# Kernel optimization log

Hardware: AMD Instinct MI355X
Metric: run time of the kernel (lower is better)

Reference implementation:

```python
import jax, jax.numpy as jnp
import numpy as np

N, E, F, H, C, G = 50000, 600000, 128, 128, 10, 500
NUM_GIN = 3
BN_EPS = 1e-5


def _bn(x, gamma, beta):
    # BatchNorm1d in training mode: batch statistics over node/graph dim
    m = jnp.mean(x, axis=0)
    v = jnp.mean((x - m) ** 2, axis=0)
    return (x - m) * jax.lax.rsqrt(v + BN_EPS) * gamma + beta


def setup_inputs() -> dict:
    key = jax.random.key(0)
    ks = jax.random.split(key, 16)
    s = 1.0 / np.sqrt(H)
    inp = {
        "x": jax.random.normal(ks[0], (N, F), dtype=jnp.float32),
        "edge_index": jax.random.randint(ks[1], (2, E), 0, N),
        "batch": jnp.sort(jax.random.randint(ks[2], (N,), 0, G)),
        # bn_feat
        "gamma_feat": jnp.ones((F,), jnp.float32),
        "beta_feat": jnp.full((F,), 1e-4, jnp.float32),
        # conv_feat (GCNConv gfn=True -> pure linear)
        "W_feat": jax.random.uniform(ks[3], (F, H), jnp.float32, -s, s),
        "b_feat": jnp.zeros((H,), jnp.float32),
        # GIN conv MLPs, stacked over 3 layers
        "gin_W1": jax.random.uniform(ks[4], (NUM_GIN, H, H), jnp.float32, -s, s),
        "gin_b1": jnp.zeros((NUM_GIN, H), jnp.float32),
        "gin_gamma": jnp.ones((NUM_GIN, H), jnp.float32),
        "gin_beta": jnp.full((NUM_GIN, H), 1e-4, jnp.float32),
        "gin_W2": jax.random.uniform(ks[5], (NUM_GIN, H, H), jnp.float32, -s, s),
        "gin_b2": jnp.zeros((NUM_GIN, H), jnp.float32),
        # one FC block (num_fc_layers=2 -> 1 bn+lin)
        "gamma_fc": jnp.ones((H,), jnp.float32),
        "beta_fc": jnp.full((H,), 1e-4, jnp.float32),
        "W_fc": jax.random.uniform(ks[6], (H, H), jnp.float32, -s, s),
        "b_fc": jnp.zeros((H,), jnp.float32),
        # bn_hidden + classifier
        "gamma_h": jnp.ones((H,), jnp.float32),
        "beta_h": jnp.full((H,), 1e-4, jnp.float32),
        "W_cls": jax.random.uniform(ks[7], (H, C), jnp.float32, -s, s),
        "b_cls": jnp.zeros((C,), jnp.float32),
    }
    return inp


def reference(x, gamma_feat, beta_feat, W_feat, b_feat,
              gin_W1, gin_b1, gin_gamma, gin_beta, gin_W2, gin_b2,
              gamma_fc, beta_fc, W_fc, b_fc,
              gamma_h, beta_h, W_cls, b_cls,
              edge_index, batch):
    src, dst = edge_index[0], edge_index[1]
    h = _bn(x, gamma_feat, beta_feat)
    h = jax.nn.relu(h @ W_feat + b_feat)  # GCNConv gfn=True == Linear
    for i in range(NUM_GIN):
        # GIN aggregation: (1+eps)*x + sum_{j->i} x_j, eps=0
        agg = jnp.zeros_like(h).at[dst].add(h[src])
        z = h + agg
        z = jax.nn.relu(_bn(z @ gin_W1[i] + gin_b1[i], gin_gamma[i], gin_beta[i]))
        h = jax.nn.relu(z @ gin_W2[i] + gin_b2[i])
    g = jax.ops.segment_sum(h, batch, num_segments=G)  # global_add_pool -> [G,H]
    g = jax.nn.relu(_bn(g, gamma_fc, beta_fc) @ W_fc + b_fc)
    g = _bn(g, gamma_h, beta_h)
    logits = g @ W_cls + b_cls
    return jax.nn.log_softmax(logits, axis=-1)
```

## Files before the change

### kernel.cpp

```cpp
#include <hip/hip_runtime.h>
#include <math.h>

#define N_NODES 50000
#define N_EDGES 600000
#define HDIM 128
#define NCLS 10
#define NGRAPH 500
#define BN_EPS 1e-5f
#define SCAN_BLOCKS 196

typedef short bf16x8 __attribute__((ext_vector_type(8)));
typedef float f32x4 __attribute__((ext_vector_type(4)));

__global__ void colstats_kernel(const float* __restrict__ X, int M, float* __restrict__ stats) {
    int col = threadIdx.x & 127;
    int sub = threadIdx.x >> 7;
    float s = 0.f, sq = 0.f;
    for (int r = blockIdx.x * 2 + sub; r < M; r += gridDim.x * 2) {
        float v = X[(size_t)r * HDIM + col];
        s += v; sq += v * v;
    }
    atomicAdd(&stats[col], s);
    atomicAdd(&stats[HDIM + col], sq);
}

__global__ void hist_kernel(const int* __restrict__ ei, int* __restrict__ counts) {
    int e = blockIdx.x * 256 + threadIdx.x;
    if (e < N_EDGES) atomicAdd(&counts[ei[N_EDGES + e]], 1);
}

__global__ __launch_bounds__(256) void scan1_kernel(const int* __restrict__ counts,
                                                    int* __restrict__ partial,
                                                    int* __restrict__ blockSums) {
    __shared__ int tmp[256];
    int tid = threadIdx.x;
    int i = blockIdx.x * 256 + tid;
    int v = (i < N_NODES) ? counts[i] : 0;
    tmp[tid] = v;
    __syncthreads();
#pragma unroll
    for (int off = 1; off < 256; off <<= 1) {
        int t = (tid >= off) ? tmp[tid - off] : 0;
        __syncthreads();
        tmp[tid] += t;
        __syncthreads();
    }
    if (i < N_NODES) partial[i] = tmp[tid] - v;
    if (tid == 255) blockSums[blockIdx.x] = tmp[255];
}

__global__ __launch_bounds__(256) void scan2_kernel(const int* __restrict__ blockSums,
                                                    int* __restrict__ blockBase) {
    __shared__ int tmp[256];
    int tid = threadIdx.x;
    int v = (tid < SCAN_BLOCKS) ? blockSums[tid] : 0;
    tmp[tid] = v;
    __syncthreads();
#pragma unroll
    for (int off = 1; off < 256; off <<= 1) {
        int t = (tid >= off) ? tmp[tid - off] : 0;
        __syncthreads();
        tmp[tid] += t;
        __syncthreads();
    }
    if (tid < SCAN_BLOCKS) blockBase[tid] = tmp[tid] - v;
}

__global__ __launch_bounds__(256) void scan3_kernel(const int* __restrict__ partial,
                                                    const int* __restrict__ blockBase,
                                                    int* __restrict__ offsets,
                                                    int* __restrict__ cursor) {
    int i = blockIdx.x * 256 + threadIdx.x;
    if (i < N_NODES) {
        int o = partial[i] + blockBase[blockIdx.x];
        offsets[i] = o;
        cursor[i] = o;
    }
    if (i == 0) offsets[N_NODES] = N_EDGES;
}

__global__ void fill_kernel(const int* __restrict__ ei, int* __restrict__ cursor, int* __restrict__ csr) {
    int e = blockIdx.x * 256 + threadIdx.x;
    if (e < N_EDGES) {
        int d = ei[N_EDGES + e];
        int pos = atomicAdd(&cursor[d], 1);
        csr[pos] = ei[e];
    }
}

__global__ __launch_bounds__(256) void agg_kernel(const float* __restrict__ h,
                                                  const int* __restrict__ offsets,
                                                  const int* __restrict__ csr,
                                                  float* __restrict__ z) {
    int node = (blockIdx.x * 256 + threadIdx.x) >> 6;
    int lane = threadIdx.x & 63;
    if (node >= N_NODES) return;
    int c0 = lane * 2;
    int beg = offsets[node], end = offsets[node + 1];
    const float2 self = *(const float2*)&h[(size_t)node * HDIM + c0];
    float ax = self.x, ay = self.y;
    for (int j = beg; j < end; j += 64) {
        int cnt = min(64, end - j);
        int sl = (j + lane < end) ? csr[j + lane] : 0;
        int t = 0;
        for (; t + 4 <= cnt; t += 4) {
            int s0 = __shfl(sl, t, 64);
            int s1 = __shfl(sl, t + 1, 64);
            int s2 = __shfl(sl, t + 2, 64);
            int s3 = __shfl(sl, t + 3, 64);
            float2 v0 = *(const float2*)&h[(size_t)s0 * HDIM + c0];
            float2 v1 = *(const float2*)&h[(size_t)s1 * HDIM + c0];
            float2 v2 = *(const float2*)&h[(size_t)s2 * HDIM + c0];
            float2 v3 = *(const float2*)&h[(size_t)s3 * HDIM + c0];
            ax += v0.x + v1.x + v2.x + v3.x;
            ay += v0.y + v1.y + v2.y + v3.y;
        }
        for (; t < cnt; t++) {
            int s = __shfl(sl, t, 64);
            float2 hv = *(const float2*)&h[(size_t)s * HDIM + c0];
            ax += hv.x; ay += hv.y;
        }
    }
    float2 o; o.x = ax; o.y = ay;
    *(float2*)&z[(size_t)node * HDIM + c0] = o;
}

__global__ __launch_bounds__(128) void segsum2_kernel(const float* __restrict__ h,
                                                      const int* __restrict__ batch,
                                                      float* __restrict__ g) {
    int b = blockIdx.x;
    int tid = threadIdx.x;
    __shared__ int bounds[2];
    if (tid < 2) {
        int target = b + tid;
        int lo = 0, hi = N_NODES;
        while (lo < hi) {
            int mid = (lo + hi) >> 1;
            if (batch[mid] < target) lo = mid + 1; else hi = mid;
        }
        bounds[tid] = lo;
    }
    __syncthreads();
    int beg = bounds[0], end = bounds[1];
    float s = 0.f;
    for (int r = beg; r < end; r++) s += h[(size_t)r * HDIM + tid];
    g[b * HDIM + tid] = s;
}

__device__ inline void dekker_split(float v, unsigned short& hi, unsigned short& lo) {
    unsigned u = __float_as_uint(v);
    hi = (unsigned short)(u >> 16);
    float flo = v - __uint_as_float(u & 0xffff0000u);
    lo = (unsigned short)(__float_as_uint(flo) >> 16);
}

__device__ inline void fragmajor_decode(int i, int& k, int& n) {
    int j = i & 7, l = (i >> 3) & 63, c = (i >> 9) & 7, s = (i >> 12) & 3;
    n = c * 16 + (l & 15);
    k = s * 32 + (l >> 4) * 8 + j;
}

__global__ __launch_bounds__(256) void prep_w(const float* __restrict__ W1,
                                              const float* __restrict__ W2,
                                              unsigned short* __restrict__ wh,
                                              unsigned short* __restrict__ wl) {
    int m = blockIdx.x;
    const float* src = (m < 3) ? (W1 + m * HDIM * HDIM) : (W2 + (m - 3) * HDIM * HDIM);
    unsigned short* dh = wh + m * HDIM * HDIM;
    unsigned short* dl = wl + m * HDIM * HDIM;
    for (int i = threadIdx.x; i < HDIM * HDIM; i += 256) {
        int k, n;
        fragmajor_decode(i, k, n);
        unsigned short h16, l16;
        dekker_split(src[k * HDIM + n], h16, l16);
        dh[i] = h16; dl[i] = l16;
    }
}

__global__ __launch_bounds__(256) void prep_feat(const float* __restrict__ W,
                                                 const float* __restrict__ bfeat,
                                                 const float* __restrict__ stats,
                                                 const float* __restrict__ gamma,
                                                 const float* __restrict__ beta,
                                                 float invCnt,
                                                 unsigned short* __restrict__ dh,
                                                 unsigned short* __restrict__ dl,
                                                 float* __restrict__ biasF) {
    __shared__ float aP[HDIM], bP[HDIM];
    int tid = threadIdx.x;
    if (tid < HDIM) {
        float m = stats[tid] * invCnt;
        float v = stats[HDIM + tid] * invCnt - m * m;
        float a = gamma[tid] * rsqrtf(v + BN_EPS);
        aP[tid] = a;
        bP[tid] = beta[tid] - m * a;
    }
    __syncthreads();
    for (int i = tid; i < HDIM * HDIM; i += 256) {
        int k, n;
        fragmajor_decode(i, k, n);
        unsigned short h16, l16;
        dekker_split(aP[k] * W[k * HDIM + n], h16, l16);
        dh[i] = h16; dl[i] = l16;
    }
    if (tid < HDIM) {
        float acc = bfeat[tid];
        for (int k = 0; k < HDIM; k++) acc = fmaf(bP[k], W[k * HDIM + tid], acc);
        biasF[tid] = acc;
    }
}

template <int MODE>
__global__ __launch_bounds__(256, 2) void mfma_gemm(const float* __restrict__ A,
                                                    const unsigned short* __restrict__ Bh,
                                                    const unsigned short* __restrict__ Bl,
                                                    const float* __restrict__ bias,
                                                    float* __restrict__ C, int M,
                                                    const float* __restrict__ statsPre,
                                                    const float* __restrict__ gammaPre,
                                                    const float* __restrict__ betaPre,
                                                    float invCnt,
                                                    float* __restrict__ statsOut) {
    __shared__ unsigned short sBfrag[32768];
    __shared__ float sA[HDIM], sBp[HDIM];
    const int tid = threadIdx.x;
    const int w = tid >> 6, l = tid & 63;
    const int q = l >> 4, c16 = l & 15;
    const int rb = blockIdx.x * 64 + w * 16;

    const int rowA = min(rb + c16, M - 1);
    const float* ap = A + (size_t)rowA * HDIM + q * 8;
    float4 araw[4][2];
#pragma unroll
    for (int s = 0; s < 4; s++) {
        araw[s][0] = *(const float4*)(ap + s * 32);
        araw[s][1] = *(const float4*)(ap + s * 32 + 4);
    }

    {
        const float4* gh = (const float4*)Bh;
        const float4* gl = (const float4*)Bl;
        float4* sh = (float4*)sBfrag;
#pragma unroll
        for (int i = 0; i < 8; i++) sh[tid + i * 256] = gh[tid + i * 256];
#pragma unroll
        for (int i = 0; i < 8; i++) sh[2048 + tid + i * 256] = gl[tid + i * 256];
    }
    if (MODE == 2) {
        if (tid < HDIM) {
            float m = statsPre[tid] * invCnt;
            float var = statsPre[HDIM + tid] * invCnt - m * m;
            float a = gammaPre[tid] * rsqrtf(var + BN_EPS);
            sA[tid] = a;
            sBp[tid] = betaPre[tid] - m * a;
        }
    }
    __syncthreads();

    f32x4 acc[8];
#pragma unroll
    for (int c = 0; c < 8; c++) acc[c] = (f32x4){0.f, 0.f, 0.f, 0.f};

#pragma unroll
    for (int s = 0; s < 4; s++) {
        const int k0 = s * 32 + q * 8;
        float vv[8] = {araw[s][0].x, araw[s][0].y, araw[s][0].z, araw[s][0].w,
                       araw[s][1].x, araw[s][1].y, araw[s][1].z, araw[s][1].w};
        bf16x8 ah, al;
#pragma unroll
        for (int j = 0; j < 8; j++) {
            float v = vv[j];
            if (MODE == 2) v = fmaxf(fmaf(v, sA[k0 + j], sBp[k0 + j]), 0.f);
            unsigned u = __float_as_uint(v);
            ah[j] = (short)(u >> 16);
            float flo = v - __uint_as_float(u & 0xffff0000u);
            al[j] = (short)(__float_as_uint(flo) >> 16);
        }
#pragma unroll
        for (int c = 0; c < 8; c++) {
            const int t = s * 8 + c;
            const int fo = (t * 64 + l) * 8;
            bf16x8 bh = *(const bf16x8*)&sBfrag[fo];
            bf16x8 bl = *(const bf16x8*)&sBfrag[16384 + fo];
            f32x4 a0 = __builtin_amdgcn_mfma_f32_16x16x32_bf16(ah, bh, acc[c], 0, 0, 0);
            a0 = __builtin_amdgcn_mfma_f32_16x16x32_bf16(al, bh, a0, 0, 0, 0);
            a0 = __builtin_amdgcn_mfma_f32_16x16x32_bf16(ah, bl, a0, 0, 0, 0);
            acc[c] = a0;
        }
    }

    float bsv[8];
#pragma unroll
    for (int c = 0; c < 8; c++) bsv[c] = bias[c * 16 + c16];
    float ssum[8], ssq[8];
    if (MODE == 1) {
#pragma unroll
        for (int c = 0; c < 8; c++) { ssum[c] = 0.f; ssq[c] = 0.f; }
    }
#pragma unroll
    for (int reg = 0; reg < 4; reg++) {
        int row = rb + q * 4 + reg;
        if (row < M) {
            float* cp = C + (size_t)row * HDIM + c16;
#pragma unroll
            for (int c = 0; c < 8; c++) {
                float v = acc[c][reg] + bsv[c];
                if (MODE != 1) v = fmaxf(v, 0.f);
                cp[c * 16] = v;
                if (MODE == 1) { ssum[c] += v; ssq[c] += v * v; }
            }
        }
    }
    if (MODE == 1) {
#pragma unroll
        for (int c = 0; c < 8; c++) {
            float s2 = ssum[c] + __shfl_xor(ssum[c], 16, 64);
            float s4 = s2 + __shfl_xor(s2, 32, 64);
            float t2 = ssq[c] + __shfl_xor(ssq[c], 16, 64);
            float t4 = t2 + __shfl_xor(t2, 32, 64);
            if (q == 0) {
                atomicAdd(&statsOut[c * 16 + c16], s4);
                atomicAdd(&statsOut[HDIM + c * 16 + c16], t4);
            }
        }
    }
}

template <bool PRE_A, bool PRE_B, bool RELU, bool STATS>
__global__ __launch_bounds__(256, 3) void gemm_bn(const float* A, const float* __restrict__ B,
                                                  const float* __restrict__ bias, float* C, int M,
                                                  const float* __restrict__ statsPre,
                                                  const float* __restrict__ gammaPre,
                                                  const float* __restrict__ betaPre,
                                                  float invCnt, float* __restrict__ statsOut) {
    __shared__ float At[64][65];
    __shared__ float Bs[64][128];
    __shared__ float aPre[128], bPre[128];

    const int tid = threadIdx.x;
    const int tx = tid & 15, ty = tid >> 4;
    const int r0 = blockIdx.x * 64;

    if (PRE_A || PRE_B) {
        if (tid < 128) {
            float m = statsPre[tid] * invCnt;
            float v = statsPre[128 + tid] * invCnt - m * m;
            float a = gammaPre[tid] * rsqrtf(v + BN_EPS);
            aPre[tid] = a;
            bPre[tid] = betaPre[tid] - m * a;
        }
        __syncthreads();
    }

    float acc[4][8];
#pragma unroll
    for (int i = 0; i < 4; i++)
#pragma unroll
        for (int j = 0; j < 8; j++) acc[i][j] = 0.f;

    float biasEff[8];
#pragma unroll
    for (int j = 0; j < 8; j++) biasEff[j] = bias[8 * tx + j];
    if (PRE_B) {
        for (int k = 0; k < 128; k++) {
            float bb = bPre[k];
            const float* Brow = B + (size_t)k * HDIM + 8 * tx;
#pragma unroll
            for (int j = 0; j < 8; j++) biasEff[j] = fmaf(bb, Brow[j], biasEff[j]);
        }
    }

    for (int kc = 0; kc < 128; kc += 64) {
#pragma unroll
        for (int i = 0; i < 4; i++) {
            int f4 = tid + i * 256;
            int row = f4 >> 4;
            int kg = f4 & 15;
            int grow = r0 + row;
            float4 av;
            if (grow < M) av = *(const float4*)(A + (size_t)grow * HDIM + kc + kg * 4);
            else av = make_float4(0.f, 0.f, 0.f, 0.f);
            if (PRE_A) {
                int kb = kc + kg * 4;
                av.x = fmaxf(fmaf(av.x, aPre[kb + 0], bPre[kb + 0]), 0.f);
                av.y = fmaxf(fmaf(av.y, aPre[kb + 1], bPre[kb + 1]), 0.f);
                av.z = fmaxf(fmaf(av.z, aPre[kb + 2], bPre[kb + 2]), 0.f);
                av.w = fmaxf(fmaf(av.w, aPre[kb + 3], bPre[kb + 3]), 0.f);
            }
            At[kg * 4 + 0][row] = av.x;
            At[kg * 4 + 1][row] = av.y;
            At[kg * 4 + 2][row] = av.z;
            At[kg * 4 + 3][row] = av.w;
        }
#pragma unroll
        for (int i = 0; i < 8; i++) {
            int f4 = tid + i * 256;
            int krow = f4 >> 5;
            int cg = f4 & 31;
            float4 bv = *(const float4*)(B + (size_t)(kc + krow) * HDIM + cg * 4);
            if (PRE_B) {
                float s = aPre[kc + krow];
                bv.x *= s; bv.y *= s; bv.z *= s; bv.w *= s;
            }
            *(float4*)&Bs[krow][cg * 4] = bv;
        }
        __syncthreads();
#pragma unroll 8
        for (int k = 0; k < 64; k++) {
            float av[4];
            av[0] = At[k][ty];
            av[1] = At[k][ty + 16];
            av[2] = At[k][ty + 32];
            av[3] = At[k][ty + 48];
            const float4 b0 = *(const float4*)&Bs[k][8 * tx];
            const float4 b1 = *(const float4*)&Bs[k][8 * tx + 4];
            float bv[8] = {b0.x, b0.y, b0.z, b0.w, b1.x, b1.y, b1.z, b1.w};
#pragma unroll
            for (int i = 0; i < 4; i++)
#pragma unroll
                for (int j = 0; j < 8; j++) acc[i][j] = fmaf(av[i], bv[j], acc[i][j]);
        }
        __syncthreads();
    }

    float s[8], sq[8];
    if (STATS) {
#pragma unroll
        for (int j = 0; j < 8; j++) { s[j] = 0.f; sq[j] = 0.f; }
    }
#pragma unroll
    for (int i = 0; i < 4; i++) {
        int grow = r0 + ty + 16 * i;
        if (grow < M) {
            float v[8];
#pragma unroll
            for (int j = 0; j < 8; j++) {
                v[j] = acc[i][j] + biasEff[j];
                if (RELU) v[j] = fmaxf(v[j], 0.f);
                if (STATS) { s[j] += v[j]; sq[j] += v[j] * v[j]; }
            }
            float4 o0 = make_float4(v[0], v[1], v[2], v[3]);
            float4 o1 = make_float4(v[4], v[5], v[6], v[7]);
            *(float4*)(C + (size_t)grow * HDIM + 8 * tx) = o0;
            *(float4*)(C + (size_t)grow * HDIM + 8 * tx + 4) = o1;
        }
    }
    if (STATS) {
        float* red = &At[0][0];
#pragma unroll
        for (int j = 0; j < 8; j++) {
            red[ty * 128 + 8 * tx + j] = s[j];
            red[2048 + ty * 128 + 8 * tx + j] = sq[j];
        }
        __syncthreads();
        if (tid < 128) {
            float t = 0.f;
#pragma unroll
            for (int u = 0; u < 16; u++) t += red[u * 128 + tid];
            atomicAdd(&statsOut[tid], t);
        } else {
            int col = tid - 128;
            float t = 0.f;
#pragma unroll
            for (int u = 0; u < 16; u++) t += red[2048 + u * 128 + col];
            atomicAdd(&statsOut[128 + col], t);
        }
    }
}

__global__ __launch_bounds__(256) void head_kernel(const float* __restrict__ g2,
                                                   const float* __restrict__ stats,
                                                   const float* __restrict__ gamma,
                                                   const float* __restrict__ beta,
                                                   const float* __restrict__ Wc,
                                                   const float* __restrict__ bc,
                                                   float* __restrict__ out, float invCnt) {
    __shared__ float Wf[HDIM * NCLS];
    __shared__ float bf[NCLS];
    __shared__ float aP[HDIM], bP[HDIM];
    const int tid = threadIdx.x;
    if (tid < HDIM) {
        float m = stats[tid] * invCnt;
        float v = stats[HDIM + tid] * invCnt - m * m;
        float a = gamma[tid] * rsqrtf(v + BN_EPS);
        aP[tid] = a;
        bP[tid] = beta[tid] - m * a;
    }
    __syncthreads();
    for (int idx = tid; idx < HDIM * NCLS; idx += 256) {
        int k = idx / NCLS;
        Wf[idx] = aP[k] * Wc[idx];
    }
    if (tid < NCLS) {
        float sv = bc[tid];
        for (int k = 0; k < HDIM; k++) sv = fmaf(bP[k], Wc[k * NCLS + tid], sv);
        bf[tid] = sv;
    }
    __syncthreads();
    int row = blockIdx.x * 256 + tid;
    if (row >= NGRAPH) return;
    float l[NCLS];
#pragma unroll
    for (int c = 0; c < NCLS; c++) l[c] = bf[c];
    for (int k = 0; k < HDIM; k++) {
        float gv = g2[row * HDIM + k];
#pragma unroll
        for (int c = 0; c < NCLS; c++) l[c] = fmaf(gv, Wf[k * NCLS + c], l[c]);
    }
    float mx = l[0];
#pragma unroll
    for (int c = 1; c < NCLS; c++) mx = fmaxf(mx, l[c]);
    float se = 0.f;
#pragma unroll
    for (int c = 0; c < NCLS; c++) se += expf(l[c] - mx);
    float lse = mx + logf(se);
#pragma unroll
    for (int c = 0; c < NCLS; c++) out[row * NCLS + c] = l[c] - lse;
}

extern "C" void kernel_launch(void* const* d_in, const int* in_sizes, int n_in,
                              void* d_out, int out_size, void* d_ws, size_t ws_size,
                              hipStream_t stream) {
    const float* x          = (const float*)d_in[0];
    const int*   ei         = (const int*)d_in[1];
    const int*   batch      = (const int*)d_in[2];
    const float* gamma_feat = (const float*)d_in[3];
    const float* beta_feat  = (const float*)d_in[4];
    const float* W_feat     = (const float*)d_in[5];
    const float* b_feat     = (const float*)d_in[6];
    const float* gin_W1     = (const float*)d_in[7];
    const float* gin_b1     = (const float*)d_in[8];
    const float* gin_gamma  = (const float*)d_in[9];
    const float* gin_beta   = (const float*)d_in[10];
    const float* gin_W2     = (const float*)d_in[11];
    const float* gin_b2     = (const float*)d_in[12];
    const float* gamma_fc   = (const float*)d_in[13];
    const float* beta_fc    = (const float*)d_in[14];
    const float* W_fc       = (const float*)d_in[15];
    const float* b_fc       = (const float*)d_in[16];
    const float* gamma_h    = (const float*)d_in[17];
    const float* beta_h     = (const float*)d_in[18];
    const float* W_cls      = (const float*)d_in[19];
    const float* b_cls      = (const float*)d_in[20];
    float* out = (float*)d_out;

    float* ws = (float*)d_ws;
    size_t off = 0;
    float* h  = ws + off; off += (size_t)N_NODES * HDIM;
    float* zy = ws + off; off += (size_t)N_NODES * HDIM;
    float* g2 = ws + off; off += NGRAPH * HDIM;
    float* g  = ws + off; off += NGRAPH * HDIM;
    size_t zstart = off;
    float* stats = ws + off; off += 256 * 6;
    int* counts = (int*)(ws + off); off += N_NODES;
    size_t zbytes = (off - zstart) * sizeof(float);
    int* offsets   = (int*)(ws + off); off += N_NODES + 1;
    int* cursor    = (int*)(ws + off); off += N_NODES;
    int* csr       = (int*)(ws + off); off += N_EDGES;
    int* partial   = (int*)(ws + off); off += N_NODES;
    int* blockSums = (int*)(ws + off); off += 256;
    int* blockBase = (int*)(ws + off); off += 256;
    off = (off + 3) & ~(size_t)3;
    unsigned short* wt_hi = (unsigned short*)(ws + off); off += 7 * HDIM * HDIM / 2;
    unsigned short* wt_lo = (unsigned short*)(ws + off); off += 7 * HDIM * HDIM / 2;
    float* biasF = ws + off; off += HDIM;

    float* statsX  = stats;
    float* statsYa[3] = {stats + 256, stats + 512, stats + 768};
    float* statsG  = stats + 1024;
    float* statsG2 = stats + 1280;

    hipMemsetAsync(stats, 0, zbytes, stream);

    const float invN = 1.f / (float)N_NODES;
    const float invG = 1.f / (float)NGRAPH;
    const int eblocks = (N_EDGES + 255) / 256;
    const int nwaves  = (N_NODES * 64 + 255) / 256;
    const int mblocks = (N_NODES + 63) / 64;

    prep_w<<<6, 256, 0, stream>>>(gin_W1, gin_W2, wt_hi, wt_lo);
    colstats_kernel<<<256, 256, 0, stream>>>(x, N_NODES, statsX);
    hist_kernel<<<eblocks, 256, 0, stream>>>(ei, counts);
    scan1_kernel<<<SCAN_BLOCKS, 256, 0, stream>>>(counts, partial, blockSums);
    scan2_kernel<<<1, 256, 0, stream>>>(blockSums, blockBase);
    scan3_kernel<<<SCAN_BLOCKS, 256, 0, stream>>>(partial, blockBase, offsets, cursor);
    fill_kernel<<<eblocks, 256, 0, stream>>>(ei, cursor, csr);
    prep_feat<<<1, 256, 0, stream>>>(W_feat, b_feat, statsX, gamma_feat, beta_feat, invN,
                                     wt_hi + 6 * HDIM * HDIM, wt_lo + 6 * HDIM * HDIM, biasF);

    mfma_gemm<0><<<mblocks, 256, 0, stream>>>(
        x, wt_hi + 6 * HDIM * HDIM, wt_lo + 6 * HDIM * HDIM, biasF, h, N_NODES,
        nullptr, nullptr, nullptr, invN, nullptr);

    for (int i = 0; i < 3; i++) {
        agg_kernel<<<nwaves, 256, 0, stream>>>(h, offsets, csr, zy);
        mfma_gemm<1><<<mblocks, 256, 0, stream>>>(
            zy, wt_hi + i * HDIM * HDIM, wt_lo + i * HDIM * HDIM, gin_b1 + i * HDIM,
            zy, N_NODES, nullptr, nullptr, nullptr, invN, statsYa[i]);
        mfma_gemm<2><<<mblocks, 256, 0, stream>>>(
            zy, wt_hi + (3 + i) * HDIM * HDIM, wt_lo + (3 + i) * HDIM * HDIM, gin_b2 + i * HDIM,
            h, N_NODES, statsYa[i], gin_gamma + i * HDIM, gin_beta + i * HDIM, invN, nullptr);
    }

    segsum2_kernel<<<NGRAPH, 128, 0, stream>>>(h, batch, g);
    colstats_kernel<<<8, 256, 0, stream>>>(g, NGRAPH, statsG);
    gemm_bn<false, true, true, true><<<(NGRAPH + 63) / 64, 256, 0, stream>>>(
        g, W_fc, b_fc, g2, NGRAPH, statsG, gamma_fc, beta_fc, invG, statsG2);
    head_kernel<<<2, 256, 0, stream>>>(g2, statsG2, gamma_h, beta_h, W_cls, b_cls, out, invG);
}
```

Before: 756.9 us.

## Make MFMA GEMM persistent with register-resident weight fragments per column half

The node GEMM now launches a fixed grid of 512 blocks that loop over 16-row tiles. Each wave keeps the bf16 hi/lo fragments for its 64-column half in registers instead of staging all weights in shared memory. This removes the per-block 64KB LDS weight copy and its occupancy limit, and spreads the weight loads over several tiles. In exchange each A row tile is loaded by two waves, register pressure rises, and an extra block barrier is added in the in-place mode 1 path.

```diff
diff --git a/kernel.cpp b/kernel.cpp
--- a/kernel.cpp
+++ b/kernel.cpp
@@ -8,6 +8,9 @@
 #define NGRAPH 500
 #define BN_EPS 1e-5f
 #define SCAN_BLOCKS 196
+#define NTILES 3125
+#define GBLK 512
+#define NITER 4
 
 typedef short bf16x8 __attribute__((ext_vector_type(8)));
 typedef float f32x4 __attribute__((ext_vector_type(4)));
@@ -215,37 +218,19 @@
                                                     const unsigned short* __restrict__ Bh,
                                                     const unsigned short* __restrict__ Bl,
                                                     const float* __restrict__ bias,
-                                                    float* __restrict__ C, int M,
+                                                    float* __restrict__ C,
                                                     const float* __restrict__ statsPre,
                                                     const float* __restrict__ gammaPre,
                                                     const float* __restrict__ betaPre,
                                                     float invCnt,
                                                     float* __restrict__ statsOut) {
-    __shared__ unsigned short sBfrag[32768];
     __shared__ float sA[HDIM], sBp[HDIM];
     const int tid = threadIdx.x;
     const int w = tid >> 6, l = tid & 63;
     const int q = l >> 4, c16 = l & 15;
-    const int rb = blockIdx.x * 64 + w * 16;
-
-    const int rowA = min(rb + c16, M - 1);
-    const float* ap = A + (size_t)rowA * HDIM + q * 8;
-    float4 araw[4][2];
-#pragma unroll
-    for (int s = 0; s < 4; s++) {
-        araw[s][0] = *(const float4*)(ap + s * 32);
-        araw[s][1] = *(const float4*)(ap + s * 32 + 4);
-    }
-
-    {
-        const float4* gh = (const float4*)Bh;
-        const float4* gl = (const float4*)Bl;
-        float4* sh = (float4*)sBfrag;
-#pragma unroll
-        for (int i = 0; i < 8; i++) sh[tid + i * 256] = gh[tid + i * 256];
-#pragma unroll
-        for (int i = 0; i < 8; i++) sh[2048 + tid + i * 256] = gl[tid + i * 256];
-    }
+    const int colHalf = w & 1, pairId = w >> 1;
+    const int colBase = colHalf * 64;
+
     if (MODE == 2) {
         if (tid < HDIM) {
             float m = statsPre[tid] * invCnt;
@@ -254,73 +239,97 @@
             sA[tid] = a;
             sBp[tid] = betaPre[tid] - m * a;
         }
-    }
-    __syncthreads();
-
-    f32x4 acc[8];
-#pragma unroll
-    for (int c = 0; c < 8; c++) acc[c] = (f32x4){0.f, 0.f, 0.f, 0.f};
-
-#pragma unroll
-    for (int s = 0; s < 4; s++) {
-        const int k0 = s * 32 + q * 8;
-        float vv[8] = {araw[s][0].x, araw[s][0].y, araw[s][0].z, araw[s][0].w,
-                       araw[s][1].x, araw[s][1].y, araw[s][1].z, araw[s][1].w};
-        bf16x8 ah, al;
-#pragma unroll
-        for (int j = 0; j < 8; j++) {
-            float v = vv[j];
-            if (MODE == 2) v = fmaxf(fmaf(v, sA[k0 + j], sBp[k0 + j]), 0.f);
-            unsigned u = __float_as_uint(v);
-            ah[j] = (short)(u >> 16);
-            float flo = v - __uint_as_float(u & 0xffff0000u);
-            al[j] = (short)(__float_as_uint(flo) >> 16);
-        }
-#pragma unroll
-        for (int c = 0; c < 8; c++) {
-            const int t = s * 8 + c;
-            const int fo = (t * 64 + l) * 8;
-            bf16x8 bh = *(const bf16x8*)&sBfrag[fo];
-            bf16x8 bl = *(const bf16x8*)&sBfrag[16384 + fo];
-            f32x4 a0 = __builtin_amdgcn_mfma_f32_16x16x32_bf16(ah, bh, acc[c], 0, 0, 0);
-            a0 = __builtin_amdgcn_mfma_f32_16x16x32_bf16(al, bh, a0, 0, 0, 0);
-            a0 = __builtin_amdgcn_mfma_f32_16x16x32_bf16(ah, bl, a0, 0, 0, 0);
-            acc[c] = a0;
-        }
-    }
-
-    float bsv[8];
-#pragma unroll
-    for (int c = 0; c < 8; c++) bsv[c] = bias[c * 16 + c16];
-    float ssum[8], ssq[8];
+        __syncthreads();
+    }
+
+    bf16x8 bh[4][4], bl[4][4];
+#pragma unroll
+    for (int s = 0; s < 4; s++)
+#pragma unroll
+        for (int cl = 0; cl < 4; cl++) {
+            const size_t fo = ((size_t)(s * 8 + colHalf * 4 + cl) * 64 + l) * 8;
+            bh[s][cl] = *(const bf16x8*)(Bh + fo);
+            bl[s][cl] = *(const bf16x8*)(Bl + fo);
+        }
+
+    float bsv[4];
+#pragma unroll
+    for (int cl = 0; cl < 4; cl++) bsv[cl] = bias[colBase + cl * 16 + c16];
+
+    float ssum[4], ssq[4];
     if (MODE == 1) {
 #pragma unroll
-        for (int c = 0; c < 8; c++) { ssum[c] = 0.f; ssq[c] = 0.f; }
-    }
-#pragma unroll
-    for (int reg = 0; reg < 4; reg++) {
-        int row = rb + q * 4 + reg;
-        if (row < M) {
-            float* cp = C + (size_t)row * HDIM + c16;
-#pragma unroll
-            for (int c = 0; c < 8; c++) {
-                float v = acc[c][reg] + bsv[c];
-                if (MODE != 1) v = fmaxf(v, 0.f);
-                cp[c * 16] = v;
-                if (MODE == 1) { ssum[c] += v; ssq[c] += v * v; }
+        for (int cl = 0; cl < 4; cl++) { ssum[cl] = 0.f; ssq[cl] = 0.f; }
+    }
+
+    for (int it = 0; it < NITER; ++it) {
+        const int tile = it * (GBLK * 2) + blockIdx.x * 2 + pairId;
+        const bool live = tile < NTILES;
+        const int tt = live ? tile : NTILES - 1;
+
+        const float* ap = A + ((size_t)tt * 16 + c16) * HDIM + q * 8;
+        float4 araw[4][2];
+#pragma unroll
+        for (int s = 0; s < 4; s++) {
+            araw[s][0] = *(const float4*)(ap + s * 32);
+            araw[s][1] = *(const float4*)(ap + s * 32 + 4);
+        }
+
+        f32x4 acc[4];
+#pragma unroll
+        for (int cl = 0; cl < 4; cl++) acc[cl] = (f32x4){0.f, 0.f, 0.f, 0.f};
+
+#pragma unroll
+        for (int s = 0; s < 4; s++) {
+            const int k0 = s * 32 + q * 8;
+            float vv[8] = {araw[s][0].x, araw[s][0].y, araw[s][0].z, araw[s][0].w,
+                           araw[s][1].x, araw[s][1].y, araw[s][1].z, araw[s][1].w};
+            bf16x8 ah, al;
+#pragma unroll
+            for (int j = 0; j < 8; j++) {
+                float v = vv[j];
+                if (MODE == 2) v = fmaxf(fmaf(v, sA[k0 + j], sBp[k0 + j]), 0.f);
+                unsigned u = __float_as_uint(v);
+                ah[j] = (short)(u >> 16);
+                float flo = v - __uint_as_float(u & 0xffff0000u);
+                al[j] = (short)(__float_as_uint(flo) >> 16);
             }
-        }
-    }
+#pragma unroll
+            for (int cl = 0; cl < 4; cl++) {
+                f32x4 a0 = __builtin_amdgcn_mfma_f32_16x16x32_bf16(ah, bh[s][cl], acc[cl], 0, 0, 0);
+                a0 = __builtin_amdgcn_mfma_f32_16x16x32_bf16(al, bh[s][cl], a0, 0, 0, 0);
+                a0 = __builtin_amdgcn_mfma_f32_16x16x32_bf16(ah, bl[s][cl], a0, 0, 0, 0);
+                acc[cl] = a0;
+            }
+        }
+
+        if (MODE == 1) __syncthreads();
+
+        if (live) {
+#pragma unroll
+            for (int reg = 0; reg < 4; reg++) {
+                float* cp = C + ((size_t)tt * 16 + q * 4 + reg) * HDIM + colBase + c16;
+#pragma unroll
+                for (int cl = 0; cl < 4; cl++) {
+                    float v = acc[cl][reg] + bsv[cl];
+                    if (MODE != 1) v = fmaxf(v, 0.f);
+                    cp[cl * 16] = v;
+                    if (MODE == 1) { ssum[cl] += v; ssq[cl] += v * v; }
+                }
+            }
+        }
+    }
+
     if (MODE == 1) {
 #pragma unroll
-        for (int c = 0; c < 8; c++) {
-            float s2 = ssum[c] + __shfl_xor(ssum[c], 16, 64);
+        for (int cl = 0; cl < 4; cl++) {
+            float s2 = ssum[cl] + __shfl_xor(ssum[cl], 16, 64);
             float s4 = s2 + __shfl_xor(s2, 32, 64);
-            float t2 = ssq[c] + __shfl_xor(ssq[c], 16, 64);
+            float t2 = ssq[cl] + __shfl_xor(ssq[cl], 16, 64);
             float t4 = t2 + __shfl_xor(t2, 32, 64);
             if (q == 0) {
-                atomicAdd(&statsOut[c * 16 + c16], s4);
-                atomicAdd(&statsOut[HDIM + c * 16 + c16], t4);
+                atomicAdd(&statsOut[colBase + cl * 16 + c16], s4);
+                atomicAdd(&statsOut[HDIM + colBase + cl * 16 + c16], t4);
             }
         }
     }
@@ -576,7 +585,6 @@
     const float invG = 1.f / (float)NGRAPH;
     const int eblocks = (N_EDGES + 255) / 256;
     const int nwaves  = (N_NODES * 64 + 255) / 256;
-    const int mblocks = (N_NODES + 63) / 64;
 
     prep_w<<<6, 256, 0, stream>>>(gin_W1, gin_W2, wt_hi, wt_lo);
     colstats_kernel<<<256, 256, 0, stream>>>(x, N_NODES, statsX);
@@ -588,18 +596,18 @@
     prep_feat<<<1, 256, 0, stream>>>(W_feat, b_feat, statsX, gamma_feat, beta_feat, invN,
                                      wt_hi + 6 * HDIM * HDIM, wt_lo + 6 * HDIM * HDIM, biasF);
 
-    mfma_gemm<0><<<mblocks, 256, 0, stream>>>(
-        x, wt_hi + 6 * HDIM * HDIM, wt_lo + 6 * HDIM * HDIM, biasF, h, N_NODES,
+    mfma_gemm<0><<<GBLK, 256, 0, stream>>>(
+        x, wt_hi + 6 * HDIM * HDIM, wt_lo + 6 * HDIM * HDIM, biasF, h,
         nullptr, nullptr, nullptr, invN, nullptr);
 
     for (int i = 0; i < 3; i++) {
         agg_kernel<<<nwaves, 256, 0, stream>>>(h, offsets, csr, zy);
-        mfma_gemm<1><<<mblocks, 256, 0, stream>>>(
+        mfma_gemm<1><<<GBLK, 256, 0, stream>>>(
             zy, wt_hi + i * HDIM * HDIM, wt_lo + i * HDIM * HDIM, gin_b1 + i * HDIM,
-            zy, N_NODES, nullptr, nullptr, nullptr, invN, statsYa[i]);
-        mfma_gemm<2><<<mblocks, 256, 0, stream>>>(
+            zy, nullptr, nullptr, nullptr, invN, statsYa[i]);
+        mfma_gemm<2><<<GBLK, 256, 0, stream>>>(
             zy, wt_hi + (3 + i) * HDIM * HDIM, wt_lo + (3 + i) * HDIM * HDIM, gin_b2 + i * HDIM,
-            h, N_NODES, statsYa[i], gin_gamma + i * HDIM, gin_beta + i * HDIM, invN, nullptr);
+            h, statsYa[i], gin_gamma + i * HDIM, gin_beta + i * HDIM, invN, nullptr);
     }
 
     segsum2_kernel<<<NGRAPH, 128, 0, stream>>>(h, batch, g);
```

New measurement: 623.6 us. 1.21x faster.
